# Optimization experiments

Hardware: AMD Instinct MI355X
Metric: run time of the kernel (lower is better)

Reference implementation:

```python
import jax, jax.numpy as jnp
import numpy as np

HEADS = 16
HEAD_DIM = 64
EMB = HEADS * HEAD_DIM
MAX_REL = 512
B, L = 4, 1024


def _rel_indices(length_q, length_k):
    # Shaw-style clipped relative distance indices into the embeddings table
    dist = jnp.arange(length_k)[None, :] - jnp.arange(length_q)[:, None]
    return jnp.clip(dist, -MAX_REL, MAX_REL) + MAX_REL  # [Lq, Lk] in [0, 2*MAX_REL]


def setup_inputs() -> dict:
    key = jax.random.key(0)
    ks = jax.random.split(key, 16)
    d = {
        "query": jax.random.normal(ks[0], (B, L, EMB), jnp.float32),
        "key": jax.random.normal(ks[1], (B, L, EMB), jnp.float32),
        "value": jax.random.normal(ks[2], (B, L, EMB), jnp.float32),
        "mask": jnp.ones((B, 1, L, L), jnp.int32),
        # per-head Linear(head_dims, head_dims) weights stored torch-style [out, in]
        "Wq": jax.random.normal(ks[3], (HEAD_DIM, HEAD_DIM), jnp.float32) / np.sqrt(HEAD_DIM),
        "bq": jax.random.normal(ks[4], (HEAD_DIM,), jnp.float32) * 0.02,
        "Wk": jax.random.normal(ks[5], (HEAD_DIM, HEAD_DIM), jnp.float32) / np.sqrt(HEAD_DIM),
        "bk": jax.random.normal(ks[6], (HEAD_DIM,), jnp.float32) * 0.02,
        "Wv": jax.random.normal(ks[7], (HEAD_DIM, HEAD_DIM), jnp.float32) / np.sqrt(HEAD_DIM),
        "bv": jax.random.normal(ks[8], (HEAD_DIM,), jnp.float32) * 0.02,
        "Wfc": jax.random.normal(ks[9], (EMB, EMB), jnp.float32) / np.sqrt(EMB),
        "bfc": jax.random.normal(ks[10], (EMB,), jnp.float32) * 0.02,
        "rel_k_table": jax.random.normal(ks[11], (2 * MAX_REL + 1, HEAD_DIM), jnp.float32) * 0.02,
        "rel_v_table": jax.random.normal(ks[12], (2 * MAX_REL + 1, HEAD_DIM), jnp.float32) * 0.02,
    }
    return d


def reference(query, key, value, mask, Wq, bq, Wk, bk, Wv, bv, Wfc, bfc, rel_k_table, rel_v_table):
    b, lq, _ = query.shape
    lk = key.shape[1]
    # split heads then per-head linear projections (torch Linear: x @ W.T + b)
    q = query.reshape(b, lq, HEADS, HEAD_DIM) @ Wq.T + bq
    k = key.reshape(b, lk, HEADS, HEAD_DIM) @ Wk.T + bk
    v = value.reshape(b, lk, HEADS, HEAD_DIM) @ Wv.T + bv

    score = jnp.einsum('bqhd,bkhd->bhqk', q, k)  # [B,H,Lq,Lk]
    score = jnp.where(mask == 0, jnp.float32(-1e20), score)

    idx = _rel_indices(lq, lk)
    a_key = rel_k_table[idx]    # [Lq, Lk, D]
    a_val = rel_v_table[idx]    # [Lq, Lk, D]
    score = score + jnp.einsum('blhd,lrd->bhlr', q, a_key)

    attn = jax.nn.softmax(score / np.sqrt(HEAD_DIM), axis=-1)

    out = jnp.einsum('bhqv,bvhd->bqhd', attn, v)
    # original: einsum('brhl,hld->bhrd', attn[b,h,q,k], a_val[q,k,d]) -> [b,q,h,d]
    out = out + jnp.einsum('bhql,qld->bqhd', attn, a_val)
    out = out.reshape(b, lq, EMB)
    return out @ Wfc.T + bfc
```

## Files before the change

### kernel.cpp

```cpp
#include <hip/hip_runtime.h>
#include <hip/hip_bf16.h>
#include <hip/hip_fp16.h>

#define SEQ 1024
#define HEADS 16
#define HDIM 64
#define EMB 1024
#define TQ 32
#define KQ 256
#define PBA_S 264
#define PBB_S 328
#define RELK_ROWS 1040
#define RELV_S 1064

typedef __bf16 bf16x8 __attribute__((ext_vector_type(8)));
typedef float floatx4 __attribute__((ext_vector_type(4)));
typedef unsigned short u16x4 __attribute__((ext_vector_type(4)));

#if __has_builtin(__builtin_amdgcn_exp2f)
#define EXP2F(x) __builtin_amdgcn_exp2f(x)
#else
#define EXP2F(x) exp2f(x)
#endif

#define QSCALE 0.18033688011112042f

static __device__ __forceinline__ unsigned short f2bu(float f) {
    __bf16 h = (__bf16)f;
    return __builtin_bit_cast(unsigned short, h);
}
static __device__ __forceinline__ float b2f(unsigned short u) {
    unsigned v = ((unsigned)u) << 16;
    return __builtin_bit_cast(float, v);
}

#define NW (1024 * 1024)
#define NRK (RELK_ROWS * 64)
#define NRV (64 * RELV_S)
#define CONVB ((NW + NRK + NRV) / 256)
#define PREPY 1626
__global__ __launch_bounds__(256) void sa_projprep_kernel(
    const float* __restrict__ qin, const float* __restrict__ kin,
    const float* __restrict__ vin,
    const float* __restrict__ Wq, const float* __restrict__ Wk,
    const float* __restrict__ Wv,
    const float* __restrict__ bq, const float* __restrict__ bk,
    const float* __restrict__ bv_,
    const float* __restrict__ Wfc, const float* __restrict__ relk,
    const float* __restrict__ relv, const int* __restrict__ mask,
    unsigned short* __restrict__ qb, unsigned short* __restrict__ kb,
    unsigned short* __restrict__ vtb,
    unsigned short* __restrict__ wfcb, unsigned short* __restrict__ relkb,
    unsigned short* __restrict__ relvtb, unsigned* __restrict__ part) {
    __shared__ unsigned wok[4];
    const int t = threadIdx.x;
    const int which = blockIdx.y;
    const int bx = blockIdx.x;

    if (bx >= 1024) {
        const int gidx = (bx - 1024) + which * PREPY;
        if (gidx < CONVB) {
            int i = gidx * 256 + t;
            if (i < NW) {
                wfcb[i] = f2bu(Wfc[i]);
            } else if (i < NW + NRK) {
                int j = i - NW;
                int r = j >> 6, d = j & 63;
                relkb[j] = (r <= 1024) ? f2bu(relk[r * 64 + d]) : 0;
            } else {
                int j = i - NW - NRK;
                int d = j / RELV_S, c = j - d * RELV_S;
                relvtb[j] = (c <= 1024) ? f2bu(relv[c * 64 + d]) : 0;
            }
        } else if (gidx < CONVB + 256) {
            const int mb = gidx - CONVB;
            const int b = mb >> 6, chunk = mb & 63;
            const int4* p = (const int4*)(mask + (size_t)b * (SEQ * SEQ) + chunk * 16384);
            int ok = 1;
#pragma unroll
            for (int i = 0; i < 16; ++i) {
                int4 v = p[t + i * 256];
                ok &= (v.x != 0 && v.y != 0 && v.z != 0 && v.w != 0) ? 1 : 0;
            }
            unsigned long long bal = __ballot(ok);
            if ((t & 63) == 0) wok[t >> 6] = (bal == ~0ull) ? 1u : 0u;
            __syncthreads();
            if (t == 0)
                part[b * 64 + chunk] = (wok[0] & wok[1] & wok[2] & wok[3]) ? 0xFFFFFFFFu : 0u;
        }
        return;
    }

    const int w = t >> 6, lane = t & 63;
    const int quad = lane >> 4, l16 = lane & 15;
    const int r0 = (bx >> 2) * 16;
    const int h = (bx & 3) * 4 + w;
    const int bidx = r0 >> 10;
    const int l0 = r0 & 1023;
    const float* x = (which == 0) ? qin : (which == 1) ? kin : vin;
    const float* Wsrc = (which == 0) ? Wq : (which == 1) ? Wk : Wv;
    const float* bias = (which == 0) ? bq : (which == 1) ? bk : bv_;

    bf16x8 wf[4][2];
#pragma unroll
    for (int dt = 0; dt < 4; ++dt)
#pragma unroll
        for (int ks = 0; ks < 2; ++ks) {
            const float* wp = Wsrc + (size_t)(dt * 16 + l16) * 64 + ks * 32 + quad * 8;
            float4 lo = *(const float4*)wp;
            float4 hi = *(const float4*)(wp + 4);
            unsigned short pw[8];
            pw[0] = f2bu(lo.x); pw[1] = f2bu(lo.y); pw[2] = f2bu(lo.z); pw[3] = f2bu(lo.w);
            pw[4] = f2bu(hi.x); pw[5] = f2bu(hi.y); pw[6] = f2bu(hi.z); pw[7] = f2bu(hi.w);
            wf[dt][ks] = *(bf16x8*)pw;
        }

    bf16x8 xf[2];
#pragma unroll
    for (int ks = 0; ks < 2; ++ks) {
        const float* xp = x + (size_t)(r0 + l16) * EMB + h * 64 + ks * 32 + quad * 8;
        float4 lo = *(const float4*)xp;
        float4 hi = *(const float4*)(xp + 4);
        unsigned short px[8];
        px[0] = f2bu(lo.x); px[1] = f2bu(lo.y); px[2] = f2bu(lo.z); px[3] = f2bu(lo.w);
        px[4] = f2bu(hi.x); px[5] = f2bu(hi.y); px[6] = f2bu(hi.z); px[7] = f2bu(hi.w);
        xf[ks] = *(bf16x8*)px;
    }
    const int bh = bidx * HEADS + h;

    if (which < 2) {
        float biasd[4];
#pragma unroll
        for (int dt = 0; dt < 4; ++dt) biasd[dt] = bias[dt * 16 + l16];
        const float sc = (which == 0) ? QSCALE : 1.0f;
        unsigned short* dst = (which == 0) ? qb : kb;
        floatx4 acc[4];
#pragma unroll
        for (int dt = 0; dt < 4; ++dt) acc[dt] = floatx4{0.f, 0.f, 0.f, 0.f};
#pragma unroll
        for (int dt = 0; dt < 4; ++dt)
#pragma unroll
            for (int ks = 0; ks < 2; ++ks)
                acc[dt] = __builtin_amdgcn_mfma_f32_16x16x32_bf16(xf[ks], wf[dt][ks], acc[dt], 0, 0, 0);
#pragma unroll
        for (int dt = 0; dt < 4; ++dt)
#pragma unroll
            for (int i = 0; i < 4; ++i) {
                const int lr = l0 + quad * 4 + i;
                float val = (acc[dt][i] + biasd[dt]) * sc;
                dst[((size_t)bh * SEQ + lr) * 64 + dt * 16 + l16] = f2bu(val);
            }
    } else {
        float biasv[4][4];
#pragma unroll
        for (int dt = 0; dt < 4; ++dt)
#pragma unroll
            for (int i = 0; i < 4; ++i) biasv[dt][i] = bias[dt * 16 + quad * 4 + i];
        floatx4 acc[4];
#pragma unroll
        for (int dt = 0; dt < 4; ++dt) acc[dt] = floatx4{0.f, 0.f, 0.f, 0.f};
#pragma unroll
        for (int dt = 0; dt < 4; ++dt)
#pragma unroll
            for (int ks = 0; ks < 2; ++ks)
                acc[dt] = __builtin_amdgcn_mfma_f32_16x16x32_bf16(wf[dt][ks], xf[ks], acc[dt], 0, 0, 0);
#pragma unroll
        for (int dt = 0; dt < 4; ++dt)
#pragma unroll
            for (int i = 0; i < 4; ++i) {
                const int d = dt * 16 + quad * 4 + i;
                float val = acc[dt][i] + biasv[dt][i];
                vtb[((size_t)bh * 64 + d) * SEQ + l0 + l16] = f2bu(val);
            }
    }
}

__global__ __launch_bounds__(512, 6) void sa_attn_kernel(
    const unsigned short* __restrict__ qb, const unsigned short* __restrict__ kb,
    const unsigned short* __restrict__ vtb, const int* __restrict__ mask,
    const unsigned short* __restrict__ relkb, const unsigned short* __restrict__ relvtb,
    const unsigned* __restrict__ part, unsigned short* __restrict__ aob) {
    __shared__ __align__(16) unsigned short PbA[TQ * PBA_S];
    __shared__ __align__(16) unsigned short PbB[TQ * PBB_S];
    __shared__ unsigned sflag;

    const int tid = threadIdx.x;
    const int w = tid >> 6, lane = tid & 63;
    const int quad = lane >> 4, l16 = lane & 15;
    const int bid = blockIdx.x;
    const int qt = bid & 31;
    const int bh = bid >> 5;
    const int q0 = qt * TQ;
    const int b = bh >> 4, h = bh & 15;

    if (tid < 64) {
        unsigned f = part[(bid >> 9) * 64 + tid];
        unsigned long long bal = __ballot(f != 0u);
        if (tid == 0) sflag = (bal == ~0ull) ? 1u : 0u;
    }

    bf16x8 aq[2][2];
#pragma unroll
    for (int rt = 0; rt < 2; ++rt) {
        const unsigned short* qrow = qb + ((size_t)bh * SEQ + q0 + rt * 16 + l16) * 64;
        aq[rt][0] = *(const bf16x8*)(qrow + quad * 8);
        aq[rt][1] = *(const bf16x8*)(qrow + 32 + quad * 8);
    }

    const int rtF = w & 1;
    const int dq = w >> 1;
    const unsigned short* vrow = vtb + ((size_t)bh * 64 + dq * 16 + l16) * SEQ;
    const unsigned short* rbase = relvtb + (size_t)(dq * 16 + l16) * RELV_S;
    const float rv0 = b2f(rbase[0]);
    const float rv1 = b2f(rbase[1024]);
    unsigned short ob[8];
#pragma unroll
    for (int j = 0; j < 8; ++j) ob[j] = 0x3F80;
    const bf16x8 onesf = *(bf16x8*)ob;

    floatx4 OaccA = {0.f, 0.f, 0.f, 0.f};
    floatx4 OaccB = {0.f, 0.f, 0.f, 0.f};
    floatx4 dnm = {0.f, 0.f, 0.f, 0.f};
    floatx4 tl = {0.f, 0.f, 0.f, 0.f};
    floatx4 th = {0.f, 0.f, 0.f, 0.f};

    __syncthreads();
    const bool mfull = (sflag != 0u);
    const int kc = w;

    for (int qu = 0; qu < 4; ++qu) {
        const int k0 = qu * KQ;
        const bool clipped = (k0 - (q0 + 31) < -512) || (k0 + 255 - q0 > 512);
        const int cmin = min(512, max(-512, k0 - (q0 + 31))) + 512;
        const int cmax = min(512, max(-512, k0 + 255 - q0)) + 512;
        const int BASE = cmin & ~15;

        if (qu) __syncthreads();

        {
            const int ct_lo = cmin >> 4, ct_hi = cmax >> 4;
            for (int ct = ct_lo + w; ct <= ct_hi; ct += 8) {
                bf16x8 bf0 = *(const bf16x8*)(relkb + (size_t)(ct * 16 + l16) * 64 + quad * 8);
                bf16x8 bf1 = *(const bf16x8*)(relkb + (size_t)(ct * 16 + l16) * 64 + 32 + quad * 8);
                floatx4 r0 = {0.f, 0.f, 0.f, 0.f}, r1 = {0.f, 0.f, 0.f, 0.f};
                r0 = __builtin_amdgcn_mfma_f32_16x16x32_bf16(bf0, aq[0][0], r0, 0, 0, 0);
                r0 = __builtin_amdgcn_mfma_f32_16x16x32_bf16(bf1, aq[0][1], r0, 0, 0, 0);
                r1 = __builtin_amdgcn_mfma_f32_16x16x32_bf16(bf0, aq[1][0], r1, 0, 0, 0);
                r1 = __builtin_amdgcn_mfma_f32_16x16x32_bf16(bf1, aq[1][1], r1, 0, 0, 0);
                const int co = ct * 16 + quad * 4 - BASE;
                u16x4 p0, p1;
#pragma unroll
                for (int i = 0; i < 4; ++i) { p0[i] = f2bu(r0[i]); p1[i] = f2bu(r1[i]); }
                *(u16x4*)&PbB[(size_t)l16 * PBB_S + co] = p0;
                *(u16x4*)&PbB[(size_t)(16 + l16) * PBB_S + co] = p1;
            }
        }
        __syncthreads();

        bf16x8 kf[2][2];
#pragma unroll
        for (int tt = 0; tt < 2; ++tt) {
            const unsigned short* krow = kb + ((size_t)bh * SEQ + k0 + kc * 32 + tt * 16 + l16) * 64;
            kf[tt][0] = *(const bf16x8*)(krow + quad * 8);
            kf[tt][1] = *(const bf16x8*)(krow + 32 + quad * 8);
        }
#pragma unroll
        for (int rt = 0; rt < 2; ++rt) {
            floatx4 a0 = {0.f, 0.f, 0.f, 0.f}, a1 = {0.f, 0.f, 0.f, 0.f};
            a0 = __builtin_amdgcn_mfma_f32_16x16x32_bf16(kf[0][0], aq[rt][0], a0, 0, 0, 0);
            a0 = __builtin_amdgcn_mfma_f32_16x16x32_bf16(kf[0][1], aq[rt][1], a0, 0, 0, 0);
            a1 = __builtin_amdgcn_mfma_f32_16x16x32_bf16(kf[1][0], aq[rt][0], a1, 0, 0, 0);
            a1 = __builtin_amdgcn_mfma_f32_16x16x32_bf16(kf[1][1], aq[rt][1], a1, 0, 0, 0);
            const unsigned short* rsrow = &PbB[(size_t)(rt * 16 + l16) * PBB_S];
            const int q = q0 + rt * 16 + l16;
            const int cb = k0 + kc * 32 - q + 512;
            u16x4 pa0, pa1;
            if (mfull) {
                if (!clipped) {
#pragma unroll
                    for (int i = 0; i < 4; ++i) {
                        pa0[i] = f2bu(EXP2F(a0[i] + b2f(rsrow[cb + quad * 4 + i - BASE])));
                        pa1[i] = f2bu(EXP2F(a1[i] + b2f(rsrow[cb + 16 + quad * 4 + i - BASE])));
                    }
                } else {
#pragma unroll
                    for (int i = 0; i < 4; ++i) {
                        const int c0 = cb + quad * 4 + i;
                        const int c1 = c0 + 16;
                        const int r0i = min(1024, max(0, c0));
                        const int r1i = min(1024, max(0, c1));
                        pa0[i] = f2bu(EXP2F(a0[i] + b2f(rsrow[r0i - BASE])));
                        pa1[i] = f2bu(EXP2F(a1[i] + b2f(rsrow[r1i - BASE])));
                    }
                }
            } else {
                const int* mrow = mask + (size_t)b * (SEQ * SEQ) + (size_t)q * SEQ;
#pragma unroll
                for (int i = 0; i < 4; ++i) {
                    const int k0i = k0 + kc * 32 + quad * 4 + i;
                    const int k1i = k0i + 16;
                    const int c0 = cb + quad * 4 + i;
                    const int c1 = c0 + 16;
                    const int r0i = min(1024, max(0, c0));
                    const int r1i = min(1024, max(0, c1));
                    float s0 = a0[i] + b2f(rsrow[r0i - BASE]);
                    float s1 = a1[i] + b2f(rsrow[r1i - BASE]);
                    s0 = (mrow[k0i] == 0) ? -1e20f : s0;
                    s1 = (mrow[k1i] == 0) ? -1e20f : s1;
                    pa0[i] = f2bu(EXP2F(s0));
                    pa1[i] = f2bu(EXP2F(s1));
                }
            }
            unsigned short* parow = &PbA[(size_t)(rt * 16 + l16) * PBA_S + kc * 32];
            *(u16x4*)(parow + quad * 4) = pa0;
            *(u16x4*)(parow + 16 + quad * 4) = pa1;
        }
        __syncthreads();

        for (int g = tid; g < TQ * (PBB_S / 8); g += 512) {
            int row = g / (PBB_S / 8), j = g - row * (PBB_S / 8);
            *(uint4*)&PbB[row * PBB_S + j * 8] = make_uint4(0u, 0u, 0u, 0u);
        }
        __syncthreads();

#pragma unroll
        for (int rt = 0; rt < 2; ++rt) {
            unsigned short* pbrow = &PbB[(size_t)(rt * 16 + l16) * PBB_S];
            const unsigned short* parow = &PbA[(size_t)(rt * 16 + l16) * PBA_S + kc * 32];
            const int cbase = k0 + kc * 32 - (q0 + rt * 16 + l16) + 512;
#pragma unroll
            for (int tt = 0; tt < 2; ++tt) {
                u16x4 pr = *(const u16x4*)(parow + tt * 16 + quad * 4);
                const int c0 = cbase + tt * 16 + quad * 4;
                if (!clipped) {
#pragma unroll
                    for (int i = 0; i < 4; ++i) pbrow[c0 + i - BASE] = pr[i];
                } else {
#pragma unroll
                    for (int i = 0; i < 4; ++i) {
                        const int c = c0 + i;
                        if ((unsigned)(c - 1) < 1023u) pbrow[c - BASE] = pr[i];
                    }
                }
            }
        }
        __syncthreads();

        {
            floatx4 accS = {0.f, 0.f, 0.f, 0.f};
            floatx4 accSI = {0.f, 0.f, 0.f, 0.f};
#pragma unroll
            for (int it = 0; it < 8; ++it) {
                const int co = it * 32 + quad * 8;
                bf16x8 ap = *(const bf16x8*)&PbA[(size_t)(rtF * 16 + l16) * PBA_S + co];
                bf16x8 bv = *(const bf16x8*)(vrow + k0 + co);
                OaccA = __builtin_amdgcn_mfma_f32_16x16x32_bf16(ap, bv, OaccA, 0, 0, 0);
                accS = __builtin_amdgcn_mfma_f32_16x16x32_bf16(ap, onesf, accS, 0, 0, 0);
            }
            const int nksB = ((cmax - BASE) >> 5) + 1;
            for (int ks = 0; ks < nksB; ++ks) {
                const int co = ks * 32 + quad * 8;
                bf16x8 ar = *(const bf16x8*)&PbB[(size_t)(rtF * 16 + l16) * PBB_S + co];
                bf16x8 br = *(const bf16x8*)(rbase + BASE + co);
                OaccB = __builtin_amdgcn_mfma_f32_16x16x32_bf16(ar, br, OaccB, 0, 0, 0);
                accSI = __builtin_amdgcn_mfma_f32_16x16x32_bf16(ar, onesf, accSI, 0, 0, 0);
            }
#pragma unroll
            for (int i = 0; i < 4; ++i) {
                dnm[i] += accS[i];
                const float tail = accS[i] - accSI[i];
                const int qi = q0 + rtF * 16 + quad * 4 + i;
                if (qi >= k0 + 512) tl[i] += tail;
                if (qi <= k0 - 257) th[i] += tail;
            }
        }
    }

#pragma unroll
    for (int i = 0; i < 4; ++i) {
        const int row = rtF * 16 + quad * 4 + i;
        const int q = q0 + row;
        const float val = (OaccA[i] + OaccB[i] + tl[i] * rv0 + th[i] * rv1) / dnm[i];
        aob[((size_t)b * SEQ + q) * EMB + h * 64 + dq * 16 + l16] = f2bu(val);
    }
}

__global__ __launch_bounds__(256, 2) void sa_fc_kernel(
    const unsigned short* __restrict__ A, const unsigned short* __restrict__ W,
    const float* __restrict__ bias, float* __restrict__ out) {
    const int t = threadIdx.x;
    const int w = t >> 6, lane = t & 63;
    const int quad = lane >> 4, l16 = lane & 15;
    const int mw = blockIdx.x * 64 + (w & 1) * 32;
    const int nw = blockIdx.y * 256 + (w >> 1) * 128;

    floatx4 acc[2][8];
#pragma unroll
    for (int mt = 0; mt < 2; ++mt)
#pragma unroll
        for (int j = 0; j < 8; ++j) acc[mt][j] = floatx4{0.f, 0.f, 0.f, 0.f};
    float bj[8];
#pragma unroll
    for (int j = 0; j < 8; ++j) bj[j] = bias[nw + j * 16 + l16];

    for (int ks = 0; ks < 32; ++ks) {
        const int co = ks * 32 + quad * 8;
        bf16x8 af0 = *(const bf16x8*)(A + (size_t)(mw + l16) * EMB + co);
        bf16x8 af1 = *(const bf16x8*)(A + (size_t)(mw + 16 + l16) * EMB + co);
#pragma unroll
        for (int j = 0; j < 8; ++j) {
            bf16x8 bf = *(const bf16x8*)(W + (size_t)(nw + j * 16 + l16) * EMB + co);
            acc[0][j] = __builtin_amdgcn_mfma_f32_16x16x32_bf16(af0, bf, acc[0][j], 0, 0, 0);
            acc[1][j] = __builtin_amdgcn_mfma_f32_16x16x32_bf16(af1, bf, acc[1][j], 0, 0, 0);
        }
    }
#pragma unroll
    for (int mt = 0; mt < 2; ++mt)
#pragma unroll
        for (int j = 0; j < 8; ++j) {
            const int col = nw + j * 16 + l16;
#pragma unroll
            for (int i = 0; i < 4; ++i) {
                const size_t row = mw + mt * 16 + quad * 4 + i;
                out[row * EMB + col] = acc[mt][j][i] + bj[j];
            }
        }
}

extern "C" void kernel_launch(void* const* d_in, const int* in_sizes, int n_in,
                              void* d_out, int out_size, void* d_ws, size_t ws_size,
                              hipStream_t stream) {
    const float* query = (const float*)d_in[0];
    const float* key = (const float*)d_in[1];
    const float* value = (const float*)d_in[2];
    const int* mask = (const int*)d_in[3];
    const float* Wq = (const float*)d_in[4];
    const float* bq = (const float*)d_in[5];
    const float* Wk = (const float*)d_in[6];
    const float* bk = (const float*)d_in[7];
    const float* Wv = (const float*)d_in[8];
    const float* bv = (const float*)d_in[9];
    const float* Wfc = (const float*)d_in[10];
    const float* bfc = (const float*)d_in[11];
    const float* relk = (const float*)d_in[12];
    const float* relv = (const float*)d_in[13];
    float* out = (float*)d_out;

    char* base = (char*)d_ws;
    const size_t MB = (size_t)1 << 20;
    unsigned short* qb = (unsigned short*)(base + 0 * MB);
    unsigned short* kb = (unsigned short*)(base + 8 * MB);
    unsigned short* vtb = (unsigned short*)(base + 16 * MB);
    unsigned short* wfcb = (unsigned short*)(base + 24 * MB);
    unsigned short* relkb = (unsigned short*)(base + 26 * MB);
    unsigned short* relvtb = (unsigned short*)(base + 26 * MB + 163840);
    unsigned* part = (unsigned*)(base + 26 * MB + 327680);
    unsigned short* aob = (unsigned short*)(base + 29 * MB);

    sa_projprep_kernel<<<dim3(1024 + PREPY, 3), 256, 0, stream>>>(
        query, key, value, Wq, Wk, Wv, bq, bk, bv,
        Wfc, relk, relv, mask, qb, kb, vtb, wfcb, relkb, relvtb, part);
    sa_attn_kernel<<<64 * 32, 512, 0, stream>>>(
        qb, kb, vtb, mask, relkb, relvtb, part, aob);
    sa_fc_kernel<<<dim3(64, 4), 256, 0, stream>>>(aob, wfcb, bfc, out);
}
```

Baseline: 492.8 us.

## Split attention over key quarters into separate blocks with a combine kernel

Each attention block now handles one 256-key quarter instead of looping over all four, which gives four times as many blocks. Each block writes fp16 partial outputs and per-row denominators, and a new combine kernel sums the partials and normalises them. Softmax has no running max, so scores get a fixed exponent bias instead. The intent is more parallelism and occupancy (launch bound 6 raised to 8) by removing the serial quarter loop and its barriers. The cost is an extra kernel, extra partial-result traffic, and repeated Q loads and relk MFMA work per block.

```diff
diff --git a/kernel.cpp b/kernel.cpp
--- a/kernel.cpp
+++ b/kernel.cpp
@@ -24,6 +24,7 @@
 #endif
 
 #define QSCALE 0.18033688011112042f
+#define PBIAS 6.0f
 
 static __device__ __forceinline__ unsigned short f2bu(float f) {
     __bf16 h = (__bf16)f;
@@ -175,11 +176,12 @@
     }
 }
 
-__global__ __launch_bounds__(512, 6) void sa_attn_kernel(
+__global__ __launch_bounds__(512, 8) void sa_attn_kernel(
     const unsigned short* __restrict__ qb, const unsigned short* __restrict__ kb,
     const unsigned short* __restrict__ vtb, const int* __restrict__ mask,
     const unsigned short* __restrict__ relkb, const unsigned short* __restrict__ relvtb,
-    const unsigned* __restrict__ part, unsigned short* __restrict__ aob) {
+    const unsigned* __restrict__ part, __half* __restrict__ Opart,
+    float* __restrict__ ms) {
     __shared__ __align__(16) unsigned short PbA[TQ * PBA_S];
     __shared__ __align__(16) unsigned short PbB[TQ * PBB_S];
     __shared__ unsigned sflag;
@@ -188,16 +190,24 @@
     const int w = tid >> 6, lane = tid & 63;
     const int quad = lane >> 4, l16 = lane & 15;
     const int bid = blockIdx.x;
-    const int qt = bid & 31;
-    const int bh = bid >> 5;
+    const int quarter = bid & 3;
+    const int qt = (bid >> 2) & 31;
+    const int bh = bid >> 7;
     const int q0 = qt * TQ;
-    const int b = bh >> 4, h = bh & 15;
+    const int k0 = quarter * KQ;
+    const int b = bh >> 4;
 
     if (tid < 64) {
-        unsigned f = part[(bid >> 9) * 64 + tid];
+        unsigned f = part[b * 64 + tid];
         unsigned long long bal = __ballot(f != 0u);
         if (tid == 0) sflag = (bal == ~0ull) ? 1u : 0u;
     }
+
+    const bool clipped = (k0 - (q0 + 31) < -512) || (k0 + 255 - q0 > 512);
+    const int cmin = min(512, max(-512, k0 - (q0 + 31))) + 512;
+    const int cmax = min(512, max(-512, k0 + 255 - q0)) + 512;
+    const int rsb = cmin & ~15;
+    const int cb0 = cmin & ~7;
 
     bf16x8 aq[2][2];
 #pragma unroll
@@ -207,182 +217,182 @@
         aq[rt][1] = *(const bf16x8*)(qrow + 32 + quad * 8);
     }
 
-    const int rtF = w & 1;
-    const int dq = w >> 1;
-    const unsigned short* vrow = vtb + ((size_t)bh * 64 + dq * 16 + l16) * SEQ;
-    const unsigned short* rbase = relvtb + (size_t)(dq * 16 + l16) * RELV_S;
-    const float rv0 = b2f(rbase[0]);
-    const float rv1 = b2f(rbase[1024]);
-    unsigned short ob[8];
-#pragma unroll
-    for (int j = 0; j < 8; ++j) ob[j] = 0x3F80;
-    const bf16x8 onesf = *(bf16x8*)ob;
-
-    floatx4 OaccA = {0.f, 0.f, 0.f, 0.f};
-    floatx4 OaccB = {0.f, 0.f, 0.f, 0.f};
-    floatx4 dnm = {0.f, 0.f, 0.f, 0.f};
-    floatx4 tl = {0.f, 0.f, 0.f, 0.f};
-    floatx4 th = {0.f, 0.f, 0.f, 0.f};
-
+    {
+        const int ct_lo = cmin >> 4, ct_hi = cmax >> 4;
+        for (int ct = ct_lo + w; ct <= ct_hi; ct += 8) {
+            bf16x8 bf0 = *(const bf16x8*)(relkb + (size_t)(ct * 16 + l16) * 64 + quad * 8);
+            bf16x8 bf1 = *(const bf16x8*)(relkb + (size_t)(ct * 16 + l16) * 64 + 32 + quad * 8);
+            floatx4 r0 = {0.f, 0.f, 0.f, 0.f}, r1 = {0.f, 0.f, 0.f, 0.f};
+            r0 = __builtin_amdgcn_mfma_f32_16x16x32_bf16(bf0, aq[0][0], r0, 0, 0, 0);
+            r0 = __builtin_amdgcn_mfma_f32_16x16x32_bf16(bf1, aq[0][1], r0, 0, 0, 0);
+            r1 = __builtin_amdgcn_mfma_f32_16x16x32_bf16(bf0, aq[1][0], r1, 0, 0, 0);
+            r1 = __builtin_amdgcn_mfma_f32_16x16x32_bf16(bf1, aq[1][1], r1, 0, 0, 0);
+            const int co = ct * 16 + quad * 4 - rsb;
+            u16x4 p0, p1;
+#pragma unroll
+            for (int i = 0; i < 4; ++i) { p0[i] = f2bu(r0[i]); p1[i] = f2bu(r1[i]); }
+            *(u16x4*)&PbB[(size_t)l16 * PBB_S + co] = p0;
+            *(u16x4*)&PbB[(size_t)(16 + l16) * PBB_S + co] = p1;
+        }
+    }
     __syncthreads();
     const bool mfull = (sflag != 0u);
+
     const int kc = w;
-
-    for (int qu = 0; qu < 4; ++qu) {
-        const int k0 = qu * KQ;
-        const bool clipped = (k0 - (q0 + 31) < -512) || (k0 + 255 - q0 > 512);
-        const int cmin = min(512, max(-512, k0 - (q0 + 31))) + 512;
-        const int cmax = min(512, max(-512, k0 + 255 - q0)) + 512;
-        const int BASE = cmin & ~15;
-
-        if (qu) __syncthreads();
-
-        {
-            const int ct_lo = cmin >> 4, ct_hi = cmax >> 4;
-            for (int ct = ct_lo + w; ct <= ct_hi; ct += 8) {
-                bf16x8 bf0 = *(const bf16x8*)(relkb + (size_t)(ct * 16 + l16) * 64 + quad * 8);
-                bf16x8 bf1 = *(const bf16x8*)(relkb + (size_t)(ct * 16 + l16) * 64 + 32 + quad * 8);
-                floatx4 r0 = {0.f, 0.f, 0.f, 0.f}, r1 = {0.f, 0.f, 0.f, 0.f};
-                r0 = __builtin_amdgcn_mfma_f32_16x16x32_bf16(bf0, aq[0][0], r0, 0, 0, 0);
-                r0 = __builtin_amdgcn_mfma_f32_16x16x32_bf16(bf1, aq[0][1], r0, 0, 0, 0);
-                r1 = __builtin_amdgcn_mfma_f32_16x16x32_bf16(bf0, aq[1][0], r1, 0, 0, 0);
-                r1 = __builtin_amdgcn_mfma_f32_16x16x32_bf16(bf1, aq[1][1], r1, 0, 0, 0);
-                const int co = ct * 16 + quad * 4 - BASE;
-                u16x4 p0, p1;
-#pragma unroll
-                for (int i = 0; i < 4; ++i) { p0[i] = f2bu(r0[i]); p1[i] = f2bu(r1[i]); }
-                *(u16x4*)&PbB[(size_t)l16 * PBB_S + co] = p0;
-                *(u16x4*)&PbB[(size_t)(16 + l16) * PBB_S + co] = p1;
-            }
-        }
-        __syncthreads();
-
-        bf16x8 kf[2][2];
+    floatx4 acc[2][2];
+#pragma unroll
+    for (int rt = 0; rt < 2; ++rt)
+#pragma unroll
+        for (int tt = 0; tt < 2; ++tt) acc[rt][tt] = floatx4{0.f, 0.f, 0.f, 0.f};
+#pragma unroll
+    for (int tt = 0; tt < 2; ++tt) {
+        const unsigned short* krow = kb + ((size_t)bh * SEQ + k0 + kc * 32 + tt * 16 + l16) * 64;
+        bf16x8 kf0 = *(const bf16x8*)(krow + quad * 8);
+        bf16x8 kf1 = *(const bf16x8*)(krow + 32 + quad * 8);
+        acc[0][tt] = __builtin_amdgcn_mfma_f32_16x16x32_bf16(kf0, aq[0][0], acc[0][tt], 0, 0, 0);
+        acc[0][tt] = __builtin_amdgcn_mfma_f32_16x16x32_bf16(kf1, aq[0][1], acc[0][tt], 0, 0, 0);
+        acc[1][tt] = __builtin_amdgcn_mfma_f32_16x16x32_bf16(kf0, aq[1][0], acc[1][tt], 0, 0, 0);
+        acc[1][tt] = __builtin_amdgcn_mfma_f32_16x16x32_bf16(kf1, aq[1][1], acc[1][tt], 0, 0, 0);
+    }
+    if (!clipped) {
+#pragma unroll
+        for (int rt = 0; rt < 2; ++rt) {
+            const unsigned short* rsrow = &PbB[(size_t)(rt * 16 + l16) * PBB_S];
+            const int cb = k0 + kc * 32 - (q0 + rt * 16 + l16) + 512 - rsb;
+#pragma unroll
+            for (int tt = 0; tt < 2; ++tt)
+#pragma unroll
+                for (int i = 0; i < 4; ++i)
+                    acc[rt][tt][i] += b2f(rsrow[cb + tt * 16 + quad * 4 + i]);
+        }
+    } else {
+#pragma unroll
+        for (int rt = 0; rt < 2; ++rt) {
+            const unsigned short* rsrow = &PbB[(size_t)(rt * 16 + l16) * PBB_S];
+            const int cb = k0 + kc * 32 - (q0 + rt * 16 + l16) + 512;
+#pragma unroll
+            for (int tt = 0; tt < 2; ++tt)
+#pragma unroll
+                for (int i = 0; i < 4; ++i) {
+                    const int c = cb + tt * 16 + quad * 4 + i;
+                    const int r = min(1024, max(0, c));
+                    acc[rt][tt][i] += b2f(rsrow[r - rsb]);
+                }
+        }
+    }
+    __syncthreads();
+
+    for (int g = tid; g < TQ * (PBB_S / 8); g += 512) {
+        int row = g / (PBB_S / 8), j = g - row * (PBB_S / 8);
+        *(uint4*)&PbB[row * PBB_S + j * 8] = make_uint4(0u, 0u, 0u, 0u);
+    }
+    __syncthreads();
+
+#pragma unroll
+    for (int rt = 0; rt < 2; ++rt) {
+        const int q = q0 + rt * 16 + l16;
+        unsigned short* parow = &PbA[(size_t)(rt * 16 + l16) * PBA_S + kc * 32];
+        unsigned short* pbrow = &PbB[(size_t)(rt * 16 + l16) * PBB_S];
+        const int cbase = k0 + kc * 32 - q + 512;
+        const int* mrow = mask + (size_t)b * (SEQ * SEQ) + (size_t)q * SEQ;
 #pragma unroll
         for (int tt = 0; tt < 2; ++tt) {
-            const unsigned short* krow = kb + ((size_t)bh * SEQ + k0 + kc * 32 + tt * 16 + l16) * 64;
-            kf[tt][0] = *(const bf16x8*)(krow + quad * 8);
-            kf[tt][1] = *(const bf16x8*)(krow + 32 + quad * 8);
-        }
-#pragma unroll
-        for (int rt = 0; rt < 2; ++rt) {
-            floatx4 a0 = {0.f, 0.f, 0.f, 0.f}, a1 = {0.f, 0.f, 0.f, 0.f};
-            a0 = __builtin_amdgcn_mfma_f32_16x16x32_bf16(kf[0][0], aq[rt][0], a0, 0, 0, 0);
-            a0 = __builtin_amdgcn_mfma_f32_16x16x32_bf16(kf[0][1], aq[rt][1], a0, 0, 0, 0);
-            a1 = __builtin_amdgcn_mfma_f32_16x16x32_bf16(kf[1][0], aq[rt][0], a1, 0, 0, 0);
-            a1 = __builtin_amdgcn_mfma_f32_16x16x32_bf16(kf[1][1], aq[rt][1], a1, 0, 0, 0);
-            const unsigned short* rsrow = &PbB[(size_t)(rt * 16 + l16) * PBB_S];
-            const int q = q0 + rt * 16 + l16;
-            const int cb = k0 + kc * 32 - q + 512;
-            u16x4 pa0, pa1;
+            u16x4 pk;
             if (mfull) {
-                if (!clipped) {
-#pragma unroll
-                    for (int i = 0; i < 4; ++i) {
-                        pa0[i] = f2bu(EXP2F(a0[i] + b2f(rsrow[cb + quad * 4 + i - BASE])));
-                        pa1[i] = f2bu(EXP2F(a1[i] + b2f(rsrow[cb + 16 + quad * 4 + i - BASE])));
-                    }
-                } else {
-#pragma unroll
-                    for (int i = 0; i < 4; ++i) {
-                        const int c0 = cb + quad * 4 + i;
-                        const int c1 = c0 + 16;
-                        const int r0i = min(1024, max(0, c0));
-                        const int r1i = min(1024, max(0, c1));
-                        pa0[i] = f2bu(EXP2F(a0[i] + b2f(rsrow[r0i - BASE])));
-                        pa1[i] = f2bu(EXP2F(a1[i] + b2f(rsrow[r1i - BASE])));
-                    }
+#pragma unroll
+                for (int i = 0; i < 4; ++i)
+                    pk[i] = f2bu(EXP2F(acc[rt][tt][i] - PBIAS));
+            } else {
+#pragma unroll
+                for (int i = 0; i < 4; ++i) {
+                    const int k = k0 + kc * 32 + tt * 16 + quad * 4 + i;
+                    float s = (mrow[k] == 0) ? -1e20f : acc[rt][tt][i];
+                    pk[i] = f2bu(EXP2F(s - PBIAS));
                 }
+            }
+            *(u16x4*)(parow + tt * 16 + quad * 4) = pk;
+            const int c0 = cbase + tt * 16 + quad * 4;
+            if (!clipped) {
+#pragma unroll
+                for (int i = 0; i < 4; ++i) pbrow[c0 + i - cb0] = pk[i];
             } else {
-                const int* mrow = mask + (size_t)b * (SEQ * SEQ) + (size_t)q * SEQ;
 #pragma unroll
                 for (int i = 0; i < 4; ++i) {
-                    const int k0i = k0 + kc * 32 + quad * 4 + i;
-                    const int k1i = k0i + 16;
-                    const int c0 = cb + quad * 4 + i;
-                    const int c1 = c0 + 16;
-                    const int r0i = min(1024, max(0, c0));
-                    const int r1i = min(1024, max(0, c1));
-                    float s0 = a0[i] + b2f(rsrow[r0i - BASE]);
-                    float s1 = a1[i] + b2f(rsrow[r1i - BASE]);
-                    s0 = (mrow[k0i] == 0) ? -1e20f : s0;
-                    s1 = (mrow[k1i] == 0) ? -1e20f : s1;
-                    pa0[i] = f2bu(EXP2F(s0));
-                    pa1[i] = f2bu(EXP2F(s1));
+                    const int c = c0 + i;
+                    if ((unsigned)(c - 1) < 1023u) pbrow[c - cb0] = pk[i];
                 }
             }
-            unsigned short* parow = &PbA[(size_t)(rt * 16 + l16) * PBA_S + kc * 32];
-            *(u16x4*)(parow + quad * 4) = pa0;
-            *(u16x4*)(parow + 16 + quad * 4) = pa1;
-        }
-        __syncthreads();
-
-        for (int g = tid; g < TQ * (PBB_S / 8); g += 512) {
-            int row = g / (PBB_S / 8), j = g - row * (PBB_S / 8);
-            *(uint4*)&PbB[row * PBB_S + j * 8] = make_uint4(0u, 0u, 0u, 0u);
-        }
-        __syncthreads();
-
-#pragma unroll
-        for (int rt = 0; rt < 2; ++rt) {
-            unsigned short* pbrow = &PbB[(size_t)(rt * 16 + l16) * PBB_S];
-            const unsigned short* parow = &PbA[(size_t)(rt * 16 + l16) * PBA_S + kc * 32];
-            const int cbase = k0 + kc * 32 - (q0 + rt * 16 + l16) + 512;
-#pragma unroll
-            for (int tt = 0; tt < 2; ++tt) {
-                u16x4 pr = *(const u16x4*)(parow + tt * 16 + quad * 4);
-                const int c0 = cbase + tt * 16 + quad * 4;
-                if (!clipped) {
-#pragma unroll
-                    for (int i = 0; i < 4; ++i) pbrow[c0 + i - BASE] = pr[i];
-                } else {
-#pragma unroll
-                    for (int i = 0; i < 4; ++i) {
-                        const int c = c0 + i;
-                        if ((unsigned)(c - 1) < 1023u) pbrow[c - BASE] = pr[i];
-                    }
-                }
-            }
-        }
-        __syncthreads();
-
-        {
-            floatx4 accS = {0.f, 0.f, 0.f, 0.f};
-            floatx4 accSI = {0.f, 0.f, 0.f, 0.f};
-#pragma unroll
-            for (int it = 0; it < 8; ++it) {
-                const int co = it * 32 + quad * 8;
-                bf16x8 ap = *(const bf16x8*)&PbA[(size_t)(rtF * 16 + l16) * PBA_S + co];
-                bf16x8 bv = *(const bf16x8*)(vrow + k0 + co);
-                OaccA = __builtin_amdgcn_mfma_f32_16x16x32_bf16(ap, bv, OaccA, 0, 0, 0);
-                accS = __builtin_amdgcn_mfma_f32_16x16x32_bf16(ap, onesf, accS, 0, 0, 0);
-            }
-            const int nksB = ((cmax - BASE) >> 5) + 1;
-            for (int ks = 0; ks < nksB; ++ks) {
-                const int co = ks * 32 + quad * 8;
-                bf16x8 ar = *(const bf16x8*)&PbB[(size_t)(rtF * 16 + l16) * PBB_S + co];
-                bf16x8 br = *(const bf16x8*)(rbase + BASE + co);
-                OaccB = __builtin_amdgcn_mfma_f32_16x16x32_bf16(ar, br, OaccB, 0, 0, 0);
-                accSI = __builtin_amdgcn_mfma_f32_16x16x32_bf16(ar, onesf, accSI, 0, 0, 0);
-            }
+        }
+    }
+    __syncthreads();
+
+    {
+        const int rt = w & 1;
+        const int dq = w >> 1;
+        floatx4 accA = {0.f, 0.f, 0.f, 0.f};
+        floatx4 accB = {0.f, 0.f, 0.f, 0.f};
+        floatx4 accS = {0.f, 0.f, 0.f, 0.f};
+        floatx4 accSI = {0.f, 0.f, 0.f, 0.f};
+        unsigned short ob[8];
+#pragma unroll
+        for (int j = 0; j < 8; ++j) ob[j] = 0x3F80;
+        const bf16x8 onesf = *(bf16x8*)ob;
+        const unsigned short* vbase = vtb + ((size_t)bh * 64 + dq * 16 + l16) * SEQ + k0;
+        const unsigned short* rbase = relvtb + (size_t)(dq * 16 + l16) * RELV_S;
+#pragma unroll
+        for (int it = 0; it < 8; ++it) {
+            const int co = it * 32 + quad * 8;
+            bf16x8 ap = *(const bf16x8*)&PbA[(size_t)(rt * 16 + l16) * PBA_S + co];
+            bf16x8 bv = *(const bf16x8*)(vbase + co);
+            accA = __builtin_amdgcn_mfma_f32_16x16x32_bf16(ap, bv, accA, 0, 0, 0);
+            accS = __builtin_amdgcn_mfma_f32_16x16x32_bf16(ap, onesf, accS, 0, 0, 0);
+        }
+        const int nksB = ((cmax - cb0) >> 5) + 1;
+        for (int ks = 0; ks < nksB; ++ks) {
+            const int co = ks * 32 + quad * 8;
+            bf16x8 ar = *(const bf16x8*)&PbB[(size_t)(rt * 16 + l16) * PBB_S + co];
+            bf16x8 br = *(const bf16x8*)(rbase + cb0 + co);
+            accB = __builtin_amdgcn_mfma_f32_16x16x32_bf16(ar, br, accB, 0, 0, 0);
+            accSI = __builtin_amdgcn_mfma_f32_16x16x32_bf16(ar, onesf, accSI, 0, 0, 0);
+        }
+        const float rv0 = b2f(rbase[0]);
+        const float rv1 = b2f(rbase[1024]);
+#pragma unroll
+        for (int i = 0; i < 4; ++i) {
+            const int row = rt * 16 + quad * 4 + i;
+            const int q = q0 + row;
+            const float tail = accS[i] - accSI[i];
+            const float lowS = (q >= k0 + 512) ? tail : 0.f;
+            const float highS = (q <= k0 - 257) ? tail : 0.f;
+            const int R = bh * SEQ + q;
+            float val = accA[i] + accB[i] + lowS * rv0 + highS * rv1;
+            Opart[((size_t)R * 4 + quarter) * 64 + dq * 16 + l16] = __float2half(val);
+        }
+        if (dq == 0 && l16 == 0) {
 #pragma unroll
             for (int i = 0; i < 4; ++i) {
-                dnm[i] += accS[i];
-                const float tail = accS[i] - accSI[i];
-                const int qi = q0 + rtF * 16 + quad * 4 + i;
-                if (qi >= k0 + 512) tl[i] += tail;
-                if (qi <= k0 - 257) th[i] += tail;
-            }
-        }
-    }
-
-#pragma unroll
-    for (int i = 0; i < 4; ++i) {
-        const int row = rtF * 16 + quad * 4 + i;
-        const int q = q0 + row;
-        const float val = (OaccA[i] + OaccB[i] + tl[i] * rv0 + th[i] * rv1) / dnm[i];
-        aob[((size_t)b * SEQ + q) * EMB + h * 64 + dq * 16 + l16] = f2bu(val);
-    }
+                const int row = rt * 16 + quad * 4 + i;
+                ms[(size_t)(bh * SEQ + q0 + row) * 4 + quarter] = accS[i];
+            }
+        }
+    }
+}
+
+__global__ __launch_bounds__(256) void sa_combine_kernel(
+    const __half* __restrict__ Opart, const float* __restrict__ ms,
+    unsigned short* __restrict__ aob) {
+    const int tid = threadIdx.x;
+    const int R = blockIdx.x * 4 + (tid >> 6);
+    const int d = tid & 63;
+    float4 dn = *(const float4*)&ms[(size_t)R * 4];
+    const float inv = 1.f / (dn.x + dn.y + dn.z + dn.w);
+    float val = 0.f;
+#pragma unroll
+    for (int j = 0; j < 4; ++j)
+        val += __half2float(Opart[((size_t)R * 4 + j) * 64 + d]);
+    val *= inv;
+    const int bh = R >> 10, q = R & 1023, b = bh >> 4, h = bh & 15;
+    aob[((size_t)b * SEQ + q) * EMB + h * 64 + d] = f2bu(val);
 }
 
 __global__ __launch_bounds__(256, 2) void sa_fc_kernel(
@@ -449,18 +459,21 @@
     char* base = (char*)d_ws;
     const size_t MB = (size_t)1 << 20;
     unsigned short* qb = (unsigned short*)(base + 0 * MB);
+    unsigned short* aob = qb;
     unsigned short* kb = (unsigned short*)(base + 8 * MB);
     unsigned short* vtb = (unsigned short*)(base + 16 * MB);
     unsigned short* wfcb = (unsigned short*)(base + 24 * MB);
     unsigned short* relkb = (unsigned short*)(base + 26 * MB);
     unsigned short* relvtb = (unsigned short*)(base + 26 * MB + 163840);
     unsigned* part = (unsigned*)(base + 26 * MB + 327680);
-    unsigned short* aob = (unsigned short*)(base + 29 * MB);
+    float* ms = (float*)(base + 27 * MB);
+    __half* Opart = (__half*)(base + 29 * MB);
 
     sa_projprep_kernel<<<dim3(1024 + PREPY, 3), 256, 0, stream>>>(
         query, key, value, Wq, Wk, Wv, bq, bk, bv,
         Wfc, relk, relv, mask, qb, kb, vtb, wfcb, relkb, relvtb, part);
-    sa_attn_kernel<<<64 * 32, 512, 0, stream>>>(
-        qb, kb, vtb, mask, relkb, relvtb, part, aob);
+    sa_attn_kernel<<<64 * 32 * 4, 512, 0, stream>>>(
+        qb, kb, vtb, mask, relkb, relvtb, part, Opart, ms);
+    sa_combine_kernel<<<(4 * HEADS * SEQ) / 4, 256, 0, stream>>>(Opart, ms, aob);
     sa_fc_kernel<<<dim3(64, 4), 256, 0, stream>>>(aob, wfcb, bfc, out);
 }
```

Result: faster. 400.6 us (-18.7%).
